# Performance work log

Measured on AMD Instinct MI355X. Metric: run time of the kernel, lower is better.

The kernel has to match this reference:

```python
import jax, jax.numpy as jnp
import numpy as np

# ---- config (mirrors conf dict passed to RegionLoss.__init__) ----
ANCHORS = jnp.array([[1.3221, 1.73145], [3.19275, 4.00944], [5.05587, 8.09892],
                     [9.47112, 4.84053], [11.2364, 10.0071]], dtype=jnp.float32)
NUM_CLASSES = 80
OBJECT_SCALE = 5.0
NO_OBJECT_SCALE = 1.0
CLASS_SCALE = 1.0
COORD_SCALE = 1.0
SIL_THRESH = 0.6
SEEN = 0  # fresh module -> seen < 12800 warm-start branch is active


def _iou_center(a, b):
    """IoU of center-format boxes (cx, cy, w, h); a, b broadcastable [..., 4]."""
    ax1, ax2 = a[..., 0] - a[..., 2] * 0.5, a[..., 0] + a[..., 2] * 0.5
    ay1, ay2 = a[..., 1] - a[..., 3] * 0.5, a[..., 1] + a[..., 3] * 0.5
    bx1, bx2 = b[..., 0] - b[..., 2] * 0.5, b[..., 0] + b[..., 2] * 0.5
    by1, by2 = b[..., 1] - b[..., 3] * 0.5, b[..., 1] + b[..., 3] * 0.5
    iw = jnp.maximum(jnp.minimum(ax2, bx2) - jnp.maximum(ax1, bx1), 0.0)
    ih = jnp.maximum(jnp.minimum(ay2, by2) - jnp.maximum(ay1, by1), 0.0)
    inter = iw * ih
    union = a[..., 2] * a[..., 3] + b[..., 2] * b[..., 3] - inter
    return inter / union


def setup_inputs() -> dict:
    key = jax.random.key(0)
    k1, k2, k3, k4 = jax.random.split(key, 4)
    B, A, C, H, W, NBOX = 32, 5, NUM_CLASSES, 52, 52, 50
    pred = jax.random.normal(k1, (B, A * (C + 5), H, W), dtype=jnp.float32)
    cls = jax.random.randint(k2, (B, NBOX, 1), 0, C).astype(jnp.float32)
    xy = jax.random.uniform(k3, (B, NBOX, 2), minval=0.02, maxval=0.98, dtype=jnp.float32)
    wh = jax.random.uniform(k4, (B, NBOX, 2), minval=0.05, maxval=0.4, dtype=jnp.float32)
    target = jnp.concatenate([cls, xy, wh], axis=-1)  # (B, NBOX, 5): cls,x,y,w,h in [0,1]
    return {"pred": pred, "target": target, "train_out": 0}


def _region_loss(pred, target):
    B, H, W = pred.shape[0], pred.shape[2], pred.shape[3]
    A, C = ANCHORS.shape[0], NUM_CLASSES
    nbox = target.shape[1]
    p = pred.reshape(B, A, C + 5, H, W)

    txy = jax.nn.sigmoid(p[:, :, 0:2])                 # (B,A,2,H,W)
    twh = p[:, :, 2:4]                                 # (B,A,2,H,W)
    pred_no_off = jnp.concatenate([txy, twh], axis=2)  # (B,A,4,H,W)
    pred_conf = jax.nn.sigmoid(p[:, :, 4])             # (B,A,H,W)
    cls_logits = p[:, :, 5:]                           # (B,A,C,H,W)

    # decode boxes to grid units (detached in the original)
    grid_x = jnp.arange(W, dtype=p.dtype)              # broadcasts along W (last dim)
    grid_y = jnp.arange(H, dtype=p.dtype)[:, None]     # broadcasts along H
    aw = ANCHORS[:, 0][None, :, None, None]
    ah = ANCHORS[:, 1][None, :, None, None]
    bx = txy[:, :, 0] + grid_x
    by = txy[:, :, 1] + grid_y
    bw = jnp.exp(twh[:, :, 0]) * aw
    bh = jnp.exp(twh[:, :, 1]) * ah
    pred_boxes = jax.lax.stop_gradient(jnp.stack([bx, by, bw, bh], axis=-1))  # (B,A,H,W,4)

    # ground truth in grid units
    scale = jnp.array([W, H, W, H], dtype=p.dtype)
    gt = target[:, :, 1:5] * scale                     # (B,nbox,4) center format
    valid = target[:, :, 1] > 0                        # sentinel: x == 0 terminates

    # conf mask: zero-out cells whose best IoU vs any GT exceeds sil_thresh
    pb_flat = pred_boxes.reshape(B, A * H * W, 4)
    ious = _iou_center(gt[:, :, None, :], pb_flat[:, None, :, :])  # (B,nbox,A*H*W)
    ious = jnp.where(valid[:, :, None], ious, 0.0)
    max_iou = jnp.max(ious, axis=1).reshape(B, A, H, W)
    conf_mask = jnp.where(max_iou > SIL_THRESH, 0.0, NO_OBJECT_SCALE)

    # best anchor per GT via width/height-only IoU (boxes at origin)
    gw, gh = gt[..., 2], gt[..., 3]
    inter = jnp.minimum(gw[..., None], ANCHORS[:, 0]) * jnp.minimum(gh[..., None], ANCHORS[:, 1])
    union = gw[..., None] * gh[..., None] + ANCHORS[:, 0] * ANCHORS[:, 1] - inter
    best_a = jnp.argmax(inter / union, axis=-1)        # (B,nbox)

    gi = jnp.clip(gt[..., 0].astype(jnp.int32), 0, W - 1)
    gj = jnp.clip(gt[..., 1].astype(jnp.int32), 0, H - 1)
    b_idx = jnp.broadcast_to(jnp.arange(B)[:, None], (B, nbox))
    bi = jnp.where(valid, b_idx, B)                    # invalid GTs -> OOB batch, dropped

    aw_b = ANCHORS[best_a, 0]
    ah_b = ANCHORS[best_a, 1]
    tx_t = gt[..., 0] - gi.astype(p.dtype)
    ty_t = gt[..., 1] - gj.astype(p.dtype)
    tw_t = jnp.log(gw / aw_b)
    th_t = jnp.log(gh / ah_b)

    pred_box_at = pred_boxes[b_idx, best_a, gj, gi]    # (B,nbox,4) decoded box at GT cell
    iou_gt = _iou_center(gt, pred_box_at)              # (B,nbox)

    # initialize targets/masks (seen < 12800 warm start)
    if SEEN < 12800:
        coord_mask = jnp.ones((B, A, H, W), dtype=p.dtype)
        target_box = jnp.zeros((B, A, 4, H, W), dtype=p.dtype).at[:, :, 0:2].set(0.5)
    else:
        coord_mask = jnp.zeros((B, A, H, W), dtype=p.dtype)
        target_box = jnp.zeros((B, A, 4, H, W), dtype=p.dtype)
    cls_mask = jnp.zeros((B, A, H, W), dtype=p.dtype)
    target_conf = jnp.zeros((B, A, H, W), dtype=p.dtype)
    target_cls = jnp.zeros((B, A, H, W), dtype=p.dtype)

    coord_mask = coord_mask.at[bi, best_a, gj, gi].set(1.0, mode='drop')
    cls_mask = cls_mask.at[bi, best_a, gj, gi].set(1.0, mode='drop')
    conf_mask = conf_mask.at[bi, best_a, gj, gi].set(OBJECT_SCALE, mode='drop')
    target_box = target_box.at[bi, best_a, 0, gj, gi].set(tx_t, mode='drop')
    target_box = target_box.at[bi, best_a, 1, gj, gi].set(ty_t, mode='drop')
    target_box = target_box.at[bi, best_a, 2, gj, gi].set(tw_t, mode='drop')
    target_box = target_box.at[bi, best_a, 3, gj, gi].set(th_t, mode='drop')
    target_conf = target_conf.at[bi, best_a, gj, gi].set(iou_gt, mode='drop')
    target_cls = target_cls.at[bi, best_a, gj, gi].set(target[:, :, 0], mode='drop')

    # losses
    half = jnp.asarray(0.5, p.dtype)
    loss_x = COORD_SCALE * jnp.sum(((pred_no_off[:, :, 0] - target_box[:, :, 0]) * coord_mask) ** 2) * half
    loss_y = COORD_SCALE * jnp.sum(((pred_no_off[:, :, 1] - target_box[:, :, 1]) * coord_mask) ** 2) * half
    loss_w = COORD_SCALE * jnp.sum(((pred_no_off[:, :, 2] - target_box[:, :, 2]) * coord_mask) ** 2) * half
    loss_h = COORD_SCALE * jnp.sum(((pred_no_off[:, :, 3] - target_box[:, :, 3]) * coord_mask) ** 2) * half
    loss_conf = jnp.sum(((pred_conf - target_conf) * jnp.sqrt(conf_mask)) ** 2) * half

    logp = jax.nn.log_softmax(cls_logits, axis=2)      # (B,A,C,H,W)
    tcls = jnp.clip(target_cls.astype(jnp.int32), 0, C - 1)
    ce = -jnp.take_along_axis(logp, tcls[:, :, None], axis=2)[:, :, 0]  # (B,A,H,W)
    loss_cls = CLASS_SCALE * jnp.sum(cls_mask * ce)

    loss = loss_x + loss_y + loss_w + loss_h + loss_conf + loss_cls
    return loss, loss_x, loss_y, loss_w, loss_h, loss_conf, loss_cls


def reference(pred, target, train_out):
    out = _region_loss(pred, target)
    if train_out:
        return out
    return out[0]
```

## Files before the change

### kernel.cpp

```cpp
#include <hip/hip_runtime.h>
#include <math.h>

#define BB 32
#define AA 5
#define CC 80
#define HH 52
#define WW 52
#define NBOX 50
#define HWSZ (HH*WW)
#define CELLS (AA*HWSZ)

__constant__ float d_aw[AA] = {1.3221f, 3.19275f, 5.05587f, 9.47112f, 11.2364f};
__constant__ float d_ah[AA] = {1.73145f, 4.00944f, 8.09892f, 4.84053f, 10.0071f};

__device__ __forceinline__ float sig(float x) { return 1.f / (1.f + expf(-x)); }


__device__ __forceinline__ void cell_of(const float* t, int& best, int& gi, int& gj, float& valid) {
    float gx = t[1] * (float)WW;
    float gy = t[2] * (float)HH;
    float gw = t[3] * (float)WW;
    float gh = t[4] * (float)HH;
    valid = (t[1] > 0.f) ? 1.f : 0.f;
    best = 0; float bestv = -1.f;
    #pragma unroll
    for (int a = 0; a < AA; ++a) {
        float inter = fminf(gw, d_aw[a]) * fminf(gh, d_ah[a]);
        float uni = gw * gh + d_aw[a] * d_ah[a] - inter;
        float r = inter / uni;
        if (r > bestv) { bestv = r; best = a; }
    }
    gi = (int)gx; gi = gi < 0 ? 0 : (gi > WW - 1 ? WW - 1 : gi);
    gj = (int)gy; gj = gj < 0 ? 0 : (gj > HH - 1 ? HH - 1 : gj);
}

__global__ void region_prep(const float* __restrict__ pred,
                            const float* __restrict__ target,
                            float4* __restrict__ boxws) {
    int b = blockIdx.x;
    int j = threadIdx.x;
    if (j >= NBOX) return;
    const float* t = target + ((size_t)b * NBOX + j) * 5;
    float gx = t[1] * (float)WW;
    float gy = t[2] * (float)HH;
    float gw = t[3] * (float)WW;
    float gh = t[4] * (float)HH;
    int best, gi, gj; float valid;
    cell_of(t, best, gi, gj, valid);

    float tx_t = gx - (float)gi;
    float ty_t = gy - (float)gj;
    float tw_t = logf(gw / d_aw[best]);
    float th_t = logf(gh / d_ah[best]);

    size_t base = ((size_t)(b * AA + best) * (CC + 5)) * HWSZ + (size_t)gj * WW + gi;
    float px = sig(pred[base]) + (float)gi;
    float py = sig(pred[base + HWSZ]) + (float)gj;
    float pw = expf(pred[base + 2 * HWSZ]) * d_aw[best];
    float ph = expf(pred[base + 3 * HWSZ]) * d_ah[best];

    float ax1 = gx - gw * 0.5f, ax2 = gx + gw * 0.5f;
    float ay1 = gy - gh * 0.5f, ay2 = gy + gh * 0.5f;
    float bx1 = px - pw * 0.5f, bx2 = px + pw * 0.5f;
    float by1 = py - ph * 0.5f, by2 = py + ph * 0.5f;
    float iw = fmaxf(fminf(ax2, bx2) - fmaxf(ax1, bx1), 0.f);
    float ih = fmaxf(fminf(ay2, by2) - fmaxf(ay1, by1), 0.f);
    float inter = iw * ih;
    float iou_gt = inter / (gw * gh + pw * ph - inter);

    float is_last = 1.f;
    for (int j2 = j + 1; j2 < NBOX; ++j2) {
        const float* t2 = target + ((size_t)b * NBOX + j2) * 5;
        int b2, i2, jj2; float v2;
        cell_of(t2, b2, i2, jj2, v2);
        if (v2 != 0.f && b2 == best && i2 == gi && jj2 == gj) is_last = 0.f;
    }

    float4* o = boxws + ((size_t)b * NBOX + j) * 4;
    if (valid != 0.f) {
        o[0] = make_float4(ax1, ax2, ay1, ay2);
        o[1] = make_float4(gw * gh, (float)best, (float)gi, (float)gj);
    } else {
        o[0] = make_float4(0.f, 0.f, 0.f, 0.f);
        o[1] = make_float4(0.f, -1.f, -1.f, -1.f);
    }
    o[2] = make_float4(tx_t, ty_t, tw_t, th_t);
    o[3] = make_float4(iou_gt, t[0], valid, is_last);
}

__device__ __forceinline__ float wave_max(float v) {
    #pragma unroll
    for (int off = 32; off > 0; off >>= 1) v = fmaxf(v, __shfl_xor(v, off, 64));
    return v;
}
__device__ __forceinline__ float wave_sum(float v) {
    #pragma unroll
    for (int off = 32; off > 0; off >>= 1) v += __shfl_xor(v, off, 64);
    return v;
}

__global__ __launch_bounds__(256) void region_ce(const float* __restrict__ pred,
                                                 const float4* __restrict__ boxws,
                                                 float* __restrict__ out) {
    int b = blockIdx.x;
    int wave = threadIdx.x >> 6;
    int lane = threadIdx.x & 63;
    float acc = 0.f;
    for (int j = wave; j < NBOX; j += 4) {
        const float4* r = boxws + ((size_t)b * NBOX + j) * 4;
        float4 r1 = r[1];
        float4 r3 = r[3];
        if (r3.z == 0.f || r3.w == 0.f) continue;
        int a = (int)r1.y, gi = (int)r1.z, gj = (int)r1.w;
        size_t cbase = ((size_t)(b * AA + a) * (CC + 5) + 5) * HWSZ + (size_t)gj * WW + gi;
        float v1 = pred[cbase + (size_t)lane * HWSZ];
        float v2 = (lane < CC - 64) ? pred[cbase + (size_t)(lane + 64) * HWSZ] : -INFINITY;
        float mx = wave_max(fmaxf(v1, v2));
        float s = expf(v1 - mx) + ((lane < CC - 64) ? expf(v2 - mx) : 0.f);
        s = wave_sum(s);
        int tcls = (int)r3.y;
        tcls = tcls < 0 ? 0 : (tcls > CC - 1 ? CC - 1 : tcls);
        float vt = ((lane == tcls) ? v1 : 0.f) + ((lane + 64 == tcls) ? v2 : 0.f);
        vt = wave_sum(vt);
        if (lane == 0) acc += (mx + logf(s)) - vt;
    }
    if (lane == 0 && acc != 0.f) atomicAdd(out, acc);
}

__global__ __launch_bounds__(256) void region_loss(const float* __restrict__ pred,
                                                   const float4* __restrict__ boxws,
                                                   float* __restrict__ out) {
    __shared__ float4 sh[NBOX * 4];
    __shared__ float wsum[4];
    int b = blockIdx.y;
    int tid = threadIdx.x;
    if (tid < NBOX * 4) sh[tid] = boxws[(size_t)b * NBOX * 4 + tid];
    __syncthreads();

    int c = blockIdx.x * 256 + tid;
    float lsum = 0.f;
    if (c < CELLS) {
        int a = c / HWSZ;
        int rem = c - a * HWSZ;
        int hh = rem / WW;
        int wwi = rem - hh * WW;
        size_t base = ((size_t)(b * AA + a) * (CC + 5)) * HWSZ + rem;
        float p0 = pred[base];
        float p1 = pred[base + HWSZ];
        float p2 = pred[base + 2 * HWSZ];
        float p3 = pred[base + 3 * HWSZ];
        float p4 = pred[base + 4 * HWSZ];
        float tx = sig(p0);
        float ty = sig(p1);
        float conf = sig(p4);
        float bx = tx + (float)wwi;
        float by = ty + (float)hh;
        float bw = expf(p2) * d_aw[a];
        float bh = expf(p3) * d_ah[a];
        float px1 = bx - bw * 0.5f, px2 = bx + bw * 0.5f;
        float py1 = by - bh * 0.5f, py2 = by + bh * 0.5f;
        float parea = bw * bh;
        float af = (float)a, wf = (float)wwi, hf = (float)hh;

        float maxiou = 0.f;
        int win = -1;
        #pragma unroll 2
        for (int j = 0; j < NBOX; ++j) {
            float4 r0 = sh[j * 4 + 0];
            float4 r1 = sh[j * 4 + 1];
            float iw = fmaxf(fminf(px2, r0.y) - fmaxf(px1, r0.x), 0.f);
            float ih = fmaxf(fminf(py2, r0.w) - fmaxf(py1, r0.z), 0.f);
            float inter = iw * ih;
            float iou = inter / (parea + r1.x - inter);
            maxiou = fmaxf(maxiou, iou);
            bool m = (r1.y == af) & (r1.z == wf) & (r1.w == hf);
            win = m ? j : win;
        }

        float dx, dy, dw, dh, lconf;
        if (win >= 0) {
            float4 r2 = sh[win * 4 + 2];
            float4 r3 = sh[win * 4 + 3];
            dx = tx - r2.x; dy = ty - r2.y; dw = p2 - r2.z; dh = p3 - r2.w;
            float d = conf - r3.x;
            lconf = 2.5f * d * d;
        } else {
            dx = tx - 0.5f; dy = ty - 0.5f; dw = p2; dh = p3;
            float cm = (maxiou > 0.6f) ? 0.f : 1.f;
            lconf = 0.5f * cm * conf * conf;
        }
        lsum = 0.5f * (dx * dx + dy * dy + dw * dw + dh * dh) + lconf;
    }

    #pragma unroll
    for (int off = 32; off > 0; off >>= 1)
        lsum += __shfl_down(lsum, off, 64);
    int wave = tid >> 6;
    if ((tid & 63) == 0) wsum[wave] = lsum;
    __syncthreads();
    if (tid == 0) {
        atomicAdd(out, wsum[0] + wsum[1] + wsum[2] + wsum[3]);
    }
}

extern "C" void kernel_launch(void* const* d_in, const int* in_sizes, int n_in,
                              void* d_out, int out_size, void* d_ws, size_t ws_size,
                              hipStream_t stream) {
    const float* pred = (const float*)d_in[0];
    const float* target = (const float*)d_in[1];
    float* out = (float*)d_out;
    float4* boxws = (float4*)d_ws;

    hipMemsetAsync(out, 0, sizeof(float) * out_size, stream);
    region_prep<<<dim3(BB), dim3(64), 0, stream>>>(pred, target, boxws);
    region_ce<<<dim3(BB), dim3(256), 0, stream>>>(pred, boxws, out);
    dim3 grid((CELLS + 255) / 256, BB);
    region_loss<<<grid, dim3(256), 0, stream>>>(pred, boxws, out);
}
```

Before: 249.1 us.

## Drop IoU division, pack GT boxes, read workspace directly, fold memset into prep

Rewrites the ignore test iou>0.6 as inter - 0.375*(parea+garea) > 0, which removes the per-box division and turns the max-IoU reduction into a max of differences. The ground-truth data is split into a compact 2-float4 box array holding a single linear cell index, so the winner match is one float compare. The main kernel reads that array straight from global memory (uniform, cached) instead of staging it in shared memory with a barrier. The output memset moves into the prep kernel, removing one launch. The algebraic rewrite of the threshold can differ from the original division form at rounding edges.

After: 254.4 us. 2.1% more time.

```diff
diff --git a/kernel.cpp b/kernel.cpp
--- a/kernel.cpp
+++ b/kernel.cpp
@@ -15,6 +15,8 @@
 
 __device__ __forceinline__ float sig(float x) { return 1.f / (1.f + expf(-x)); }
 
+#define LBOX_OFF  0
+#define WINFO_OFF (BB * NBOX * 2)
 
 __device__ __forceinline__ void cell_of(const float* t, int& best, int& gi, int& gj, float& valid) {
     float gx = t[1] * (float)WW;
@@ -36,9 +38,13 @@
 
 __global__ void region_prep(const float* __restrict__ pred,
                             const float* __restrict__ target,
-                            float4* __restrict__ boxws) {
+                            float4* __restrict__ ws,
+                            float* __restrict__ out, int out_size) {
     int b = blockIdx.x;
     int j = threadIdx.x;
+    if (b == 0 && j >= NBOX) {
+        for (int k = j - NBOX; k < out_size; k += 64 - NBOX) out[k] = 0.f;
+    }
     if (j >= NBOX) return;
     const float* t = target + ((size_t)b * NBOX + j) * 5;
     float gx = t[1] * (float)WW;
@@ -76,16 +82,18 @@
         if (v2 != 0.f && b2 == best && i2 == gi && jj2 == gj) is_last = 0.f;
     }
 
-    float4* o = boxws + ((size_t)b * NBOX + j) * 4;
+    float cellf = (float)(best * HWSZ + gj * WW + gi);
+    float4* l = ws + LBOX_OFF + ((size_t)b * NBOX + j) * 2;
     if (valid != 0.f) {
-        o[0] = make_float4(ax1, ax2, ay1, ay2);
-        o[1] = make_float4(gw * gh, (float)best, (float)gi, (float)gj);
+        l[0] = make_float4(ax1, ax2, ay1, ay2);
+        l[1] = make_float4(0.375f * gw * gh, cellf, 0.f, 0.f);
     } else {
-        o[0] = make_float4(0.f, 0.f, 0.f, 0.f);
-        o[1] = make_float4(0.f, -1.f, -1.f, -1.f);
-    }
-    o[2] = make_float4(tx_t, ty_t, tw_t, th_t);
-    o[3] = make_float4(iou_gt, t[0], valid, is_last);
+        l[0] = make_float4(0.f, 0.f, 0.f, 0.f);
+        l[1] = make_float4(0.f, -1.f, 0.f, 0.f);
+    }
+    float4* w = ws + WINFO_OFF + ((size_t)b * NBOX + j) * 2;
+    w[0] = make_float4(tx_t, ty_t, tw_t, th_t);
+    w[1] = make_float4(iou_gt, t[0], valid, is_last);
 }
 
 __device__ __forceinline__ float wave_max(float v) {
@@ -100,25 +108,27 @@
 }
 
 __global__ __launch_bounds__(256) void region_ce(const float* __restrict__ pred,
-                                                 const float4* __restrict__ boxws,
+                                                 const float4* __restrict__ ws,
                                                  float* __restrict__ out) {
     int b = blockIdx.x;
     int wave = threadIdx.x >> 6;
     int lane = threadIdx.x & 63;
     float acc = 0.f;
     for (int j = wave; j < NBOX; j += 4) {
-        const float4* r = boxws + ((size_t)b * NBOX + j) * 4;
-        float4 r1 = r[1];
-        float4 r3 = r[3];
-        if (r3.z == 0.f || r3.w == 0.f) continue;
-        int a = (int)r1.y, gi = (int)r1.z, gj = (int)r1.w;
-        size_t cbase = ((size_t)(b * AA + a) * (CC + 5) + 5) * HWSZ + (size_t)gj * WW + gi;
+        const float4* w = ws + WINFO_OFF + ((size_t)b * NBOX + j) * 2;
+        const float4* l = ws + LBOX_OFF + ((size_t)b * NBOX + j) * 2;
+        float4 w1 = w[1];
+        if (w1.z == 0.f || w1.w == 0.f) continue;
+        int cell = (int)l[1].y;
+        int a = cell / HWSZ;
+        int rem = cell - a * HWSZ;
+        size_t cbase = ((size_t)(b * AA + a) * (CC + 5) + 5) * HWSZ + rem;
         float v1 = pred[cbase + (size_t)lane * HWSZ];
         float v2 = (lane < CC - 64) ? pred[cbase + (size_t)(lane + 64) * HWSZ] : -INFINITY;
         float mx = wave_max(fmaxf(v1, v2));
         float s = expf(v1 - mx) + ((lane < CC - 64) ? expf(v2 - mx) : 0.f);
         s = wave_sum(s);
-        int tcls = (int)r3.y;
+        int tcls = (int)w1.y;
         tcls = tcls < 0 ? 0 : (tcls > CC - 1 ? CC - 1 : tcls);
         float vt = ((lane == tcls) ? v1 : 0.f) + ((lane + 64 == tcls) ? v2 : 0.f);
         vt = wave_sum(vt);
@@ -128,15 +138,11 @@
 }
 
 __global__ __launch_bounds__(256) void region_loss(const float* __restrict__ pred,
-                                                   const float4* __restrict__ boxws,
+                                                   const float4* __restrict__ ws,
                                                    float* __restrict__ out) {
-    __shared__ float4 sh[NBOX * 4];
     __shared__ float wsum[4];
     int b = blockIdx.y;
     int tid = threadIdx.x;
-    if (tid < NBOX * 4) sh[tid] = boxws[(size_t)b * NBOX * 4 + tid];
-    __syncthreads();
-
     int c = blockIdx.x * 256 + tid;
     float lsum = 0.f;
     if (c < CELLS) {
@@ -159,34 +165,34 @@
         float bh = expf(p3) * d_ah[a];
         float px1 = bx - bw * 0.5f, px2 = bx + bw * 0.5f;
         float py1 = by - bh * 0.5f, py2 = by + bh * 0.5f;
-        float parea = bw * bh;
-        float af = (float)a, wf = (float)wwi, hf = (float)hh;
-
-        float maxiou = 0.f;
+        float pa375 = 0.375f * bw * bh;
+        float cf = (float)c;
+
+        const float4* lb = ws + LBOX_OFF + (size_t)b * NBOX * 2;
+        float hit = -1.f;
         int win = -1;
-        #pragma unroll 2
+        #pragma unroll 5
         for (int j = 0; j < NBOX; ++j) {
-            float4 r0 = sh[j * 4 + 0];
-            float4 r1 = sh[j * 4 + 1];
-            float iw = fmaxf(fminf(px2, r0.y) - fmaxf(px1, r0.x), 0.f);
-            float ih = fmaxf(fminf(py2, r0.w) - fmaxf(py1, r0.z), 0.f);
+            float4 l0 = lb[j * 2 + 0];
+            float4 l1 = lb[j * 2 + 1];
+            float iw = fmaxf(fminf(px2, l0.y) - fmaxf(px1, l0.x), 0.f);
+            float ih = fmaxf(fminf(py2, l0.w) - fmaxf(py1, l0.z), 0.f);
             float inter = iw * ih;
-            float iou = inter / (parea + r1.x - inter);
-            maxiou = fmaxf(maxiou, iou);
-            bool m = (r1.y == af) & (r1.z == wf) & (r1.w == hf);
-            win = m ? j : win;
+            hit = fmaxf(hit, inter - (pa375 + l1.x));
+            win = (l1.y == cf) ? j : win;
         }
 
         float dx, dy, dw, dh, lconf;
         if (win >= 0) {
-            float4 r2 = sh[win * 4 + 2];
-            float4 r3 = sh[win * 4 + 3];
-            dx = tx - r2.x; dy = ty - r2.y; dw = p2 - r2.z; dh = p3 - r2.w;
-            float d = conf - r3.x;
+            const float4* w = ws + WINFO_OFF + ((size_t)b * NBOX + win) * 2;
+            float4 w0 = w[0];
+            float iou_gt = w[1].x;
+            dx = tx - w0.x; dy = ty - w0.y; dw = p2 - w0.z; dh = p3 - w0.w;
+            float d = conf - iou_gt;
             lconf = 2.5f * d * d;
         } else {
             dx = tx - 0.5f; dy = ty - 0.5f; dw = p2; dh = p3;
-            float cm = (maxiou > 0.6f) ? 0.f : 1.f;
+            float cm = (hit > 0.f) ? 0.f : 1.f;
             lconf = 0.5f * cm * conf * conf;
         }
         lsum = 0.5f * (dx * dx + dy * dy + dw * dw + dh * dh) + lconf;
@@ -209,11 +215,10 @@
     const float* pred = (const float*)d_in[0];
     const float* target = (const float*)d_in[1];
     float* out = (float*)d_out;
-    float4* boxws = (float4*)d_ws;
-
-    hipMemsetAsync(out, 0, sizeof(float) * out_size, stream);
-    region_prep<<<dim3(BB), dim3(64), 0, stream>>>(pred, target, boxws);
-    region_ce<<<dim3(BB), dim3(256), 0, stream>>>(pred, boxws, out);
+    float4* ws = (float4*)d_ws;
+
+    region_prep<<<dim3(BB), dim3(64), 0, stream>>>(pred, target, ws, out, out_size);
+    region_ce<<<dim3(BB), dim3(256), 0, stream>>>(pred, ws, out);
     dim3 grid((CELLS + 255) / 256, BB);
-    region_loss<<<grid, dim3(256), 0, stream>>>(pred, boxws, out);
-}
+    region_loss<<<grid, dim3(256), 0, stream>>>(pred, ws, out);
+}
```
